# Optimization experiments

Hardware: AMD Instinct MI355X
Metric: run time of the kernel (lower is better)

Reference implementation:

```python
import jax, jax.numpy as jnp
import numpy as np

NEG = -9e15

def setup_inputs() -> dict:
    key = jax.random.key(0)
    k1, k2, k3, k4, k5 = jax.random.split(key, 5)
    N, Fin, Fout = 8192, 256, 128
    h = jax.random.normal(k1, (N, Fin), dtype=jnp.float32)
    adj = jax.random.randint(k2, (N, N), 0, 2, dtype=jnp.int32)
    # Parameters (xavier_uniform with gain=1.414 for a1/a2; kaiming-like for W is fine as random init)
    lim_w = float(np.sqrt(6.0 / (Fin + Fout)))
    W = jax.random.uniform(k3, (Fout, Fin), dtype=jnp.float32, minval=-lim_w, maxval=lim_w)
    lim_a = float(1.414 * np.sqrt(6.0 / (Fout + 1)))
    a1 = jax.random.uniform(k4, (Fout, 1), dtype=jnp.float32, minval=-lim_a, maxval=lim_a)
    a2 = jax.random.uniform(k5, (Fout, 1), dtype=jnp.float32, minval=-lim_a, maxval=lim_a)
    return {"h": h, "adj": adj, "W": W, "a1": a1, "a2": a2}

def reference(h, adj, W, a1, a2):
    Wh = h @ W.T                                   # [N, Fout]
    s1 = (Wh @ a1)                                 # [N, 1]
    s2 = (Wh @ a2)                                 # [N, 1]
    e = jax.nn.leaky_relu(s1 + s2.T, 0.2)          # [N, N]
    att = jnp.where(adj > 0, e, jnp.float32(NEG))
    att = jax.nn.softmax(att, axis=1)
    h_prime = att @ Wh                             # [N, Fout]
    return jax.nn.elu(h_prime)
```

## Files before the change

### kernel.cpp

```cpp
#include <hip/hip_runtime.h>
#include <cstdint>
#include <cstddef>

#define N_NODES 8192
#define FIN 256
#define FOUT 128
#define MT 32
#define KC 256
#define JS 2
#define JW (N_NODES / JS)
#define NCHS (JW / KC)
#define LOG2E 1.4426950408889634f

typedef __attribute__((ext_vector_type(8))) short bf16x8;
typedef __attribute__((ext_vector_type(4))) float f32x4;
typedef __attribute__((ext_vector_type(4))) int i32x4;
typedef __attribute__((ext_vector_type(2))) unsigned int u32x2;

__device__ __forceinline__ float bf2f(unsigned short u) {
    union { unsigned int i; float f; } v; v.i = ((unsigned int)u) << 16; return v.f;
}
__device__ __forceinline__ unsigned short f2bf(float f) {
    union { float f; unsigned int i; } v; v.f = f;
    unsigned int r = (v.i + 0x7FFFu + ((v.i >> 16) & 1u)) >> 16;
    return (unsigned short)r;
}
__device__ __forceinline__ unsigned int pack_bf16(float a, float b) {
    return (unsigned)f2bf(a) | ((unsigned)f2bf(b) << 16);
}

__device__ __forceinline__ size_t whb_idx(int j, int f) {
    return ((size_t)((j >> 5) * 8 + (f >> 4)) << 9) + (((j >> 3) & 3) << 7)
         + ((f & 15) << 3) + (j & 7);
}

__global__ __launch_bounds__(256) void wh_kernel(const float* __restrict__ h,
                                                 const float* __restrict__ W,
                                                 unsigned short* __restrict__ whB) {
    __shared__ float hT[64][FIN + 5];
    const int t = threadIdx.x;
    const int i0 = blockIdx.x * 64;
    const int f0 = blockIdx.y * 32;
#pragma unroll
    for (int c = 0; c < 16; ++c) {
        int chunk = c * 256 + t;
        int row = chunk >> 6, col = (chunk & 63) * 4;
        f32x4 v = *(const f32x4*)&h[(size_t)(i0 + row) * FIN + col];
        hT[row][col] = v[0]; hT[row][col + 1] = v[1];
        hT[row][col + 2] = v[2]; hT[row][col + 3] = v[3];
    }
    __syncthreads();
    const int lane = t & 63;
    const int fb8 = __builtin_amdgcn_readfirstlane(f0 + (t >> 6) * 8);
    const float* w0 = W + (size_t)fb8 * FIN;
    float acc[8] = {0.f, 0.f, 0.f, 0.f, 0.f, 0.f, 0.f, 0.f};
    for (int k = 0; k < FIN; k += 4) {
        float h0 = hT[lane][k],     h1 = hT[lane][k + 1];
        float h2 = hT[lane][k + 2], h3 = hT[lane][k + 3];
#pragma unroll
        for (int c = 0; c < 8; ++c) {
            const float* wr = w0 + c * FIN;
            acc[c] += h0 * wr[k] + h1 * wr[k + 1] + h2 * wr[k + 2] + h3 * wr[k + 3];
        }
    }
    const int i = i0 + lane;
#pragma unroll
    for (int c = 0; c < 8; ++c)
        whB[whb_idx(i, fb8 + c)] = f2bf(acc[c]);
}

__global__ __launch_bounds__(256) void s_kernel(const unsigned short* __restrict__ whB,
                                                const float* __restrict__ a1,
                                                const float* __restrict__ a2,
                                                float* __restrict__ s1,
                                                float* __restrict__ s2) {
    __shared__ float p1[4][64], p2[4][64];
    const int t = threadIdx.x;
    const int l = t & 63;
    const int g = t >> 6;
    const int i = blockIdx.x * 64 + l;
    float acc1 = 0.f, acc2 = 0.f;
#pragma unroll
    for (int fb = g * 2; fb < g * 2 + 2; ++fb) {
#pragma unroll
        for (int sl = 0; sl < 16; ++sl) {
            int f = fb * 16 + sl;
            float v = bf2f(whB[whb_idx(i, f)]);
            acc1 += v * a1[f];
            acc2 += v * a2[f];
        }
    }
    p1[g][l] = acc1; p2[g][l] = acc2;
    __syncthreads();
    if (g == 0) {
        s1[i] = (p1[0][l] + p1[1][l] + p1[2][l] + p1[3][l]) * LOG2E;
        s2[i] = (p2[0][l] + p2[1][l] + p2[2][l] + p2[3][l]) * LOG2E;
    }
}

__global__ __launch_bounds__(256) void gat_kernel(const int* __restrict__ adj,
                                                  const unsigned short* __restrict__ whB,
                                                  const float* __restrict__ s1,
                                                  const float* __restrict__ s2,
                                                  float* __restrict__ num0,
                                                  float* __restrict__ num1,
                                                  float* __restrict__ den0,
                                                  float* __restrict__ den1) {
    __shared__ __align__(16) unsigned short sP[MT][KC + 8];
    __shared__ float sDen[MT];
    __shared__ float sS1[MT];
    const int t = threadIdx.x;
    const int slice = blockIdx.x & 1;
    const int i0 = (blockIdx.x >> 1) * MT;
    const int jb = slice * JW;
    const int kb0 = slice * (JW / 32);
    float* __restrict__ num = slice ? num1 : num0;
    float* __restrict__ den = slice ? den1 : den0;
    if (t < MT) { sDen[t] = 0.f; sS1[t] = s1[i0 + t]; }
    __syncthreads();

    const int r0 = t >> 4;
    const int s  = t & 15;
    const int lane = t & 63;
    const int quad = lane >> 4;
    const int sl = lane & 15;
    const int wv = t >> 6;
    const int* adjRow0 = adj + (size_t)(i0 + r0) * N_NODES;
    const int* adjRow1 = adjRow0 + (size_t)16 * N_NODES;
    const float s1a = sS1[r0];
    const float s1b = sS1[r0 + 16];

    f32x4 acc00 = {0.f,0.f,0.f,0.f}, acc01 = {0.f,0.f,0.f,0.f};
    f32x4 acc10 = {0.f,0.f,0.f,0.f}, acc11 = {0.f,0.f,0.f,0.f};

    i32x4 aj0[4], aj1[4]; f32x4 sv[4];
#pragma unroll
    for (int q = 0; q < 4; ++q) {
        int col = jb + q * 64 + s * 4;
        aj0[q] = *(const i32x4*)&adjRow0[col];
        aj1[q] = *(const i32x4*)&adjRow1[col];
        sv[q]  = *(const f32x4*)&s2[col];
    }

    for (int ch = 0; ch < NCHS; ++ch) {
        float part0 = 0.f, part1 = 0.f;
#pragma unroll
        for (int q = 0; q < 4; ++q) {
            float p0[4], p1v[4];
#pragma unroll
            for (int r = 0; r < 4; ++r) {
                float y0 = s1a + sv[q][r];
                float y1 = s1b + sv[q][r];
                y0 = fmaxf(y0, 0.2f * y0);
                y1 = fmaxf(y1, 0.2f * y1);
                float e0 = __builtin_amdgcn_exp2f(y0);
                float e1 = __builtin_amdgcn_exp2f(y1);
                p0[r]  = (aj0[q][r] > 0) ? e0 : 0.f;
                p1v[r] = (aj1[q][r] > 0) ? e1 : 0.f;
                part0 += p0[r];
                part1 += p1v[r];
            }
            u32x2 pk0, pk1;
            pk0.x = pack_bf16(p0[0], p0[1]);   pk0.y = pack_bf16(p0[2], p0[3]);
            pk1.x = pack_bf16(p1v[0], p1v[1]); pk1.y = pack_bf16(p1v[2], p1v[3]);
            *(u32x2*)&sP[r0][q * 64 + s * 4] = pk0;
            *(u32x2*)&sP[r0 + 16][q * 64 + s * 4] = pk1;
        }
        if (ch + 1 < NCHS) {
            int jn = jb + (ch + 1) * KC;
#pragma unroll
            for (int q = 0; q < 4; ++q) {
                int col = jn + q * 64 + s * 4;
                aj0[q] = *(const i32x4*)&adjRow0[col];
                aj1[q] = *(const i32x4*)&adjRow1[col];
                sv[q]  = *(const f32x4*)&s2[col];
            }
        }
        part0 += __shfl_xor(part0, 1); part1 += __shfl_xor(part1, 1);
        part0 += __shfl_xor(part0, 2); part1 += __shfl_xor(part1, 2);
        part0 += __shfl_xor(part0, 4); part1 += __shfl_xor(part1, 4);
        part0 += __shfl_xor(part0, 8); part1 += __shfl_xor(part1, 8);
        if (s == 0) { sDen[r0] += part0; sDen[r0 + 16] += part1; }
        __syncthreads();
#pragma unroll
        for (int kq = 0; kq < KC / 32; ++kq) {
            bf16x8 a0  = *(const bf16x8*)&sP[sl][kq * 32 + quad * 8];
            bf16x8 a1f = *(const bf16x8*)&sP[16 + sl][kq * 32 + quad * 8];
            int kb = kb0 + ch * (KC / 32) + kq;
            const unsigned short* t0 = whB + ((size_t)(kb * 8 + wv * 2) << 9) + lane * 8;
            bf16x8 b0 = *(const bf16x8*)t0;
            bf16x8 b1 = *(const bf16x8*)(t0 + 512);
            acc00 = __builtin_amdgcn_mfma_f32_16x16x32_bf16(a0,  b0, acc00, 0, 0, 0);
            acc01 = __builtin_amdgcn_mfma_f32_16x16x32_bf16(a0,  b1, acc01, 0, 0, 0);
            acc10 = __builtin_amdgcn_mfma_f32_16x16x32_bf16(a1f, b0, acc10, 0, 0, 0);
            acc11 = __builtin_amdgcn_mfma_f32_16x16x32_bf16(a1f, b1, acc11, 0, 0, 0);
        }
        __syncthreads();
    }
    if (t < MT) den[i0 + t] = sDen[t];
#pragma unroll
    for (int m = 0; m < 2; ++m) {
#pragma unroll
        for (int nn = 0; nn < 2; ++nn) {
            f32x4 a = (m == 0) ? (nn == 0 ? acc00 : acc01) : (nn == 0 ? acc10 : acc11);
#pragma unroll
            for (int r = 0; r < 4; ++r) {
                int row = m * 16 + quad * 4 + r;
                num[(size_t)(i0 + row) * FOUT + wv * 32 + nn * 16 + sl] = a[r];
            }
        }
    }
}

__global__ __launch_bounds__(256) void fin_kernel(float* __restrict__ out,
                                                  const float* __restrict__ num1,
                                                  const float* __restrict__ den0,
                                                  const float* __restrict__ den1) {
    const int idx = blockIdx.x * 256 + threadIdx.x;
    const int i = idx >> 7;
    float numv = out[idx] + num1[idx];
    float denv = fmaxf(den0[i] + den1[i], 1e-30f);
    float v = numv / denv;
    out[idx] = (v > 0.f) ? v : expm1f(v);
}

extern "C" void kernel_launch(void* const* d_in, const int* in_sizes, int n_in,
                              void* d_out, int out_size, void* d_ws, size_t ws_size,
                              hipStream_t stream) {
    const float* h   = (const float*)d_in[0];
    const int*   adj = (const int*)d_in[1];
    const float* W   = (const float*)d_in[2];
    const float* a1  = (const float*)d_in[3];
    const float* a2  = (const float*)d_in[4];

    unsigned short* whB = (unsigned short*)d_ws;
    float* s1   = (float*)d_in[0];
    float* s2   = s1 + N_NODES;
    float* num1 = s2 + N_NODES;
    float* den0 = num1 + (size_t)N_NODES * FOUT;
    float* den1 = den0 + N_NODES;
    float* num0 = (float*)d_out;

    wh_kernel<<<dim3(N_NODES / 64, FOUT / 32), 256, 0, stream>>>(h, W, whB);
    s_kernel<<<dim3(N_NODES / 64), 256, 0, stream>>>(whB, a1, a2, s1, s2);
    gat_kernel<<<dim3((N_NODES / MT) * JS), 256, 0, stream>>>(adj, whB, s1, s2,
                                                              num0, num1, den0, den1);
    fin_kernel<<<dim3(N_NODES * FOUT / 256), 256, 0, stream>>>(num0, num1, den0, den1);
}
```

Baseline: 435.5 us.

## Pack adjacency into bitmasks in a pre-pass and split j into four slices

Adds a pack_kernel that reads the int32 adjacency once and compresses it into 64-bit ballot masks. The attention kernel then reads bits instead of int32 values, and its column-to-thread mapping changes so each thread's 16 columns sit in one 16-bit mask field. The j dimension is split into four slices instead of two, which doubles the grid and adds partial numerator buffers that the finalize kernel sums. The full adj read still happens once in the pack pass, so the saving comes mainly from the gat kernel being lighter and from more parallelism. The cost is an extra launch plus extra partial-sum traffic in workspace.

```diff
diff --git a/kernel.cpp b/kernel.cpp
--- a/kernel.cpp
+++ b/kernel.cpp
@@ -7,14 +7,13 @@
 #define FOUT 128
 #define MT 32
 #define KC 256
-#define JS 2
+#define JS 4
 #define JW (N_NODES / JS)
 #define NCHS (JW / KC)
 #define LOG2E 1.4426950408889634f
 
 typedef __attribute__((ext_vector_type(8))) short bf16x8;
 typedef __attribute__((ext_vector_type(4))) float f32x4;
-typedef __attribute__((ext_vector_type(4))) int i32x4;
 typedef __attribute__((ext_vector_type(2))) unsigned int u32x2;
 
 __device__ __forceinline__ float bf2f(unsigned short u) {
@@ -32,6 +31,33 @@
 __device__ __forceinline__ size_t whb_idx(int j, int f) {
     return ((size_t)((j >> 5) * 8 + (f >> 4)) << 9) + (((j >> 3) & 3) << 7)
          + ((f & 15) << 3) + (j & 7);
+}
+
+__global__ __launch_bounds__(256) void pack_kernel(const int* __restrict__ adj,
+                                                   unsigned long long* __restrict__ bits) {
+    const int t = threadIdx.x;
+    const int lane = t & 63;
+    const int wv = t >> 6;
+    const int wid = blockIdx.x * 4 + wv;
+#pragma unroll
+    for (int pass = 0; pass < 2; ++pass) {
+        const int row = wid + pass * 4096;
+        const int* ar = adj + (size_t)row * N_NODES;
+        unsigned long long k0 = 0, k1 = 0;
+#pragma unroll
+        for (int seg = 0; seg < 64; ++seg) {
+            unsigned long long m = __ballot(ar[seg * 64 + lane] > 0);
+            if (lane == seg) k0 = m;
+        }
+#pragma unroll
+        for (int seg = 0; seg < 64; ++seg) {
+            unsigned long long m = __ballot(ar[4096 + seg * 64 + lane] > 0);
+            if (lane == seg) k1 = m;
+        }
+        unsigned long long* br = bits + (size_t)row * 128;
+        br[lane] = k0;
+        br[64 + lane] = k1;
+    }
 }
 
 __global__ __launch_bounds__(256) void wh_kernel(const float* __restrict__ h,
@@ -98,24 +124,23 @@
     }
 }
 
-__global__ __launch_bounds__(256) void gat_kernel(const int* __restrict__ adj,
+__global__ __launch_bounds__(256) void gat_kernel(const unsigned long long* __restrict__ bits,
                                                   const unsigned short* __restrict__ whB,
                                                   const float* __restrict__ s1,
                                                   const float* __restrict__ s2,
-                                                  float* __restrict__ num0,
-                                                  float* __restrict__ num1,
-                                                  float* __restrict__ den0,
-                                                  float* __restrict__ den1) {
+                                                  float* __restrict__ out,
+                                                  float* __restrict__ nums,
+                                                  float* __restrict__ dens) {
     __shared__ __align__(16) unsigned short sP[MT][KC + 8];
     __shared__ float sDen[MT];
     __shared__ float sS1[MT];
     const int t = threadIdx.x;
-    const int slice = blockIdx.x & 1;
-    const int i0 = (blockIdx.x >> 1) * MT;
+    const int slice = blockIdx.x & (JS - 1);
+    const int i0 = (blockIdx.x >> 2) * MT;
     const int jb = slice * JW;
     const int kb0 = slice * (JW / 32);
-    float* __restrict__ num = slice ? num1 : num0;
-    float* __restrict__ den = slice ? den1 : den0;
+    float* __restrict__ num = slice ? (nums + (size_t)(slice - 1) * N_NODES * FOUT) : out;
+    float* __restrict__ den = dens + (size_t)slice * N_NODES;
     if (t < MT) { sDen[t] = 0.f; sS1[t] = s1[i0 + t]; }
     __syncthreads();
 
@@ -125,24 +150,25 @@
     const int quad = lane >> 4;
     const int sl = lane & 15;
     const int wv = t >> 6;
-    const int* adjRow0 = adj + (size_t)(i0 + r0) * N_NODES;
-    const int* adjRow1 = adjRow0 + (size_t)16 * N_NODES;
+    const unsigned long long* bRow0 = bits + (size_t)(i0 + r0) * 128;
+    const unsigned long long* bRow1 = bRow0 + (size_t)16 * 128;
+    const int shft = (s & 3) * 16;
     const float s1a = sS1[r0];
     const float s1b = sS1[r0 + 16];
 
     f32x4 acc00 = {0.f,0.f,0.f,0.f}, acc01 = {0.f,0.f,0.f,0.f};
     f32x4 acc10 = {0.f,0.f,0.f,0.f}, acc11 = {0.f,0.f,0.f,0.f};
 
-    i32x4 aj0[4], aj1[4]; f32x4 sv[4];
-#pragma unroll
-    for (int q = 0; q < 4; ++q) {
-        int col = jb + q * 64 + s * 4;
-        aj0[q] = *(const i32x4*)&adjRow0[col];
-        aj1[q] = *(const i32x4*)&adjRow1[col];
-        sv[q]  = *(const f32x4*)&s2[col];
-    }
+    int w0i = (jb >> 6) + (s >> 2);
+    unsigned long long bw0 = bRow0[w0i];
+    unsigned long long bw1 = bRow1[w0i];
+    f32x4 sv[4];
+#pragma unroll
+    for (int q = 0; q < 4; ++q) sv[q] = *(const f32x4*)&s2[jb + s * 16 + q * 4];
 
     for (int ch = 0; ch < NCHS; ++ch) {
+        unsigned int m0 = (unsigned int)(bw0 >> shft) & 0xFFFFu;
+        unsigned int m1 = (unsigned int)(bw1 >> shft) & 0xFFFFu;
         float part0 = 0.f, part1 = 0.f;
 #pragma unroll
         for (int q = 0; q < 4; ++q) {
@@ -155,26 +181,25 @@
                 y1 = fmaxf(y1, 0.2f * y1);
                 float e0 = __builtin_amdgcn_exp2f(y0);
                 float e1 = __builtin_amdgcn_exp2f(y1);
-                p0[r]  = (aj0[q][r] > 0) ? e0 : 0.f;
-                p1v[r] = (aj1[q][r] > 0) ? e1 : 0.f;
+                int b = q * 4 + r;
+                p0[r]  = ((m0 >> b) & 1u) ? e0 : 0.f;
+                p1v[r] = ((m1 >> b) & 1u) ? e1 : 0.f;
                 part0 += p0[r];
                 part1 += p1v[r];
             }
             u32x2 pk0, pk1;
             pk0.x = pack_bf16(p0[0], p0[1]);   pk0.y = pack_bf16(p0[2], p0[3]);
             pk1.x = pack_bf16(p1v[0], p1v[1]); pk1.y = pack_bf16(p1v[2], p1v[3]);
-            *(u32x2*)&sP[r0][q * 64 + s * 4] = pk0;
-            *(u32x2*)&sP[r0 + 16][q * 64 + s * 4] = pk1;
+            *(u32x2*)&sP[r0][s * 16 + q * 4] = pk0;
+            *(u32x2*)&sP[r0 + 16][s * 16 + q * 4] = pk1;
         }
         if (ch + 1 < NCHS) {
             int jn = jb + (ch + 1) * KC;
-#pragma unroll
-            for (int q = 0; q < 4; ++q) {
-                int col = jn + q * 64 + s * 4;
-                aj0[q] = *(const i32x4*)&adjRow0[col];
-                aj1[q] = *(const i32x4*)&adjRow1[col];
-                sv[q]  = *(const f32x4*)&s2[col];
-            }
+            int wni = (jn >> 6) + (s >> 2);
+            bw0 = bRow0[wni];
+            bw1 = bRow1[wni];
+#pragma unroll
+            for (int q = 0; q < 4; ++q) sv[q] = *(const f32x4*)&s2[jn + s * 16 + q * 4];
         }
         part0 += __shfl_xor(part0, 1); part1 += __shfl_xor(part1, 1);
         part0 += __shfl_xor(part0, 2); part1 += __shfl_xor(part1, 2);
@@ -213,14 +238,14 @@
 }
 
 __global__ __launch_bounds__(256) void fin_kernel(float* __restrict__ out,
-                                                  const float* __restrict__ num1,
-                                                  const float* __restrict__ den0,
-                                                  const float* __restrict__ den1) {
+                                                  const float* __restrict__ nums,
+                                                  const float* __restrict__ dens) {
     const int idx = blockIdx.x * 256 + threadIdx.x;
     const int i = idx >> 7;
-    float numv = out[idx] + num1[idx];
-    float denv = fmaxf(den0[i] + den1[i], 1e-30f);
-    float v = numv / denv;
+    const size_t NF = (size_t)N_NODES * FOUT;
+    float numv = out[idx] + nums[idx] + nums[NF + idx] + nums[2 * NF + idx];
+    float denv = dens[i] + dens[N_NODES + i] + dens[2 * N_NODES + i] + dens[3 * N_NODES + i];
+    float v = numv / fmaxf(denv, 1e-30f);
     out[idx] = (v > 0.f) ? v : expm1f(v);
 }
 
@@ -233,17 +258,19 @@
     const float* a1  = (const float*)d_in[3];
     const float* a2  = (const float*)d_in[4];
 
-    unsigned short* whB = (unsigned short*)d_ws;
-    float* s1   = (float*)d_in[0];
+    char* ws = (char*)d_ws;
+    unsigned short*     whB  = (unsigned short*)ws;
+    unsigned long long* bits = (unsigned long long*)(ws + (2u << 20));
+    float* s1   = (float*)(ws + (10u << 20));
     float* s2   = s1 + N_NODES;
-    float* num1 = s2 + N_NODES;
-    float* den0 = num1 + (size_t)N_NODES * FOUT;
-    float* den1 = den0 + N_NODES;
-    float* num0 = (float*)d_out;
-
+    float* dens = s2 + N_NODES;
+    float* nums = dens + 4 * N_NODES;
+    float* out  = (float*)d_out;
+
+    pack_kernel<<<dim3(1024), 256, 0, stream>>>(adj, bits);
     wh_kernel<<<dim3(N_NODES / 64, FOUT / 32), 256, 0, stream>>>(h, W, whB);
     s_kernel<<<dim3(N_NODES / 64), 256, 0, stream>>>(whB, a1, a2, s1, s2);
-    gat_kernel<<<dim3((N_NODES / MT) * JS), 256, 0, stream>>>(adj, whB, s1, s2,
-                                                              num0, num1, den0, den1);
-    fin_kernel<<<dim3(N_NODES * FOUT / 256), 256, 0, stream>>>(num0, num1, den0, den1);
-}
+    gat_kernel<<<dim3((N_NODES / MT) * JS), 256, 0, stream>>>(bits, whB, s1, s2,
+                                                              out, nums, dens);
+    fin_kernel<<<dim3(N_NODES * FOUT / 256), 256, 0, stream>>>(out, nums, dens);
+}
```

Measured after the change: 433.2 us. No clear change (-0.5%).
